# Performance work log

Measured on AMD Instinct MI355X. Metric: run time of the kernel, lower is better.

## Reference

```python
import jax, jax.numpy as jnp
import numpy as np

D_MODEL = 1024
N_HEADS = 16
D_K = D_MODEL // N_HEADS


def _rope_sin_cos(seq_len, d_k, dtype):
    inv_freq = 1.0 / (10000.0 ** (jnp.arange(0, d_k, 2, dtype=jnp.float32) / d_k))
    pos = jnp.arange(seq_len, dtype=jnp.float32)[:, None]          # [S,1]
    ang = pos * inv_freq[None, :]                                   # [S,d_k/2]
    sin = jnp.concatenate([jnp.sin(ang), jnp.sin(ang)], axis=-1)    # [S,d_k]
    cos = jnp.concatenate([jnp.cos(ang), jnp.cos(ang)], axis=-1)
    return sin.astype(dtype), cos.astype(dtype)


def _rotate_half(x):
    x1, x2 = jnp.split(x, 2, axis=-1)
    return jnp.concatenate([-x2, x1], axis=-1)


def _apply_rope(x, sin, cos):
    # x: [B,H,S,d_k]; sin/cos: [S,d_k] broadcast over B,H
    return x * cos[None, None] + _rotate_half(x) * sin[None, None]


def setup_inputs() -> dict:
    key = jax.random.key(0)
    ks = jax.random.split(key, 8)
    B, S = 2, 2048
    s = 1.0 / np.sqrt(D_MODEL)
    return {
        "query": jax.random.normal(ks[0], (B, S, D_MODEL), jnp.float32),
        "key": jax.random.normal(ks[1], (B, S, D_MODEL), jnp.float32),
        "value": jax.random.normal(ks[2], (B, S, D_MODEL), jnp.float32),
        "Wq": jax.random.normal(ks[3], (D_MODEL, D_MODEL), jnp.float32) * s,
        "Wk": jax.random.normal(ks[4], (D_MODEL, D_MODEL), jnp.float32) * s,
        "Wv": jax.random.normal(ks[5], (D_MODEL, D_MODEL), jnp.float32) * s,
        "Wo": jax.random.normal(ks[6], (D_MODEL, D_MODEL), jnp.float32) * s,
        "bo": jnp.zeros((D_MODEL,), jnp.float32),
    }


def reference(query, key, value, Wq, Wk, Wv, Wo, bo):
    B, Sq, _ = query.shape
    Sk = key.shape[1]
    # projections; torch Linear: x @ W.T (here W stored as [out,in])
    Q = (query @ Wq.T).reshape(B, Sq, N_HEADS, D_K).transpose(0, 2, 1, 3)
    K = (key @ Wk.T).reshape(B, Sk, N_HEADS, D_K).transpose(0, 2, 1, 3)
    V = (value @ Wv.T).reshape(B, Sk, N_HEADS, D_K).transpose(0, 2, 1, 3)
    sin_q, cos_q = _rope_sin_cos(Sq, D_K, Q.dtype)
    sin_k, cos_k = _rope_sin_cos(Sk, D_K, K.dtype)
    Q = _apply_rope(Q, sin_q, cos_q)
    K = _apply_rope(K, sin_k, cos_k)
    scores = jnp.einsum("bhqd,bhkd->bhqk", Q, K) / jnp.sqrt(jnp.asarray(D_K, Q.dtype))
    attn = jax.nn.softmax(scores, axis=-1)
    ctx = jnp.einsum("bhqk,bhkd->bhqd", attn, V)
    ctx = ctx.transpose(0, 2, 1, 3).reshape(B, Sq, D_MODEL)
    out = ctx @ Wo.T + bo
    return out, attn
```

## Files before the change

### kernel.cpp

```cpp
#include <hip/hip_runtime.h>
#include <cmath>

#define BB 2
#define SS 2048
#define DMODEL 1024
#define NHEADS 16
#define DK 64
#define BSR (BB*SS)

typedef float f32x4 __attribute__((ext_vector_type(4)));
typedef short s16x8 __attribute__((ext_vector_type(8)));
typedef unsigned short ushort_t;
#define MFMA_BF16 __builtin_amdgcn_mfma_f32_16x16x32_bf16

__device__ __forceinline__ unsigned short f2bf(float x) {
    unsigned int u = __float_as_uint(x);
    unsigned int r = u + 0x7FFFu + ((u >> 16) & 1u);
    return (unsigned short)(r >> 16);
}
__device__ __forceinline__ float bf2f(unsigned short h) {
    return __uint_as_float(((unsigned int)h) << 16);
}
__device__ __forceinline__ unsigned int pk2(float lo, float hi) {
    return (unsigned int)f2bf(lo) | ((unsigned int)f2bf(hi) << 16);
}

__device__ __forceinline__ size_t qk_idx(int bh, int s, int d) {
    return ((((size_t)bh * 128 + (s >> 4)) * 2 + (d >> 5)) * 4 + ((d >> 3) & 3)) * 128
           + (size_t)((s & 15) * 8 + (d & 7));
}
__device__ __forceinline__ size_t v_idx(int bh, int s, int d) {
    return ((((size_t)bh * 64 + (s >> 5)) * 4 + (d >> 4)) * 4 + ((s >> 3) & 3)) * 128
           + (size_t)((d & 15) * 8 + (s & 7));
}

__global__ __launch_bounds__(256)
void split_all(const float* __restrict__ q, const float* __restrict__ k,
               const float* __restrict__ v, const float* __restrict__ wq,
               const float* __restrict__ wk, const float* __restrict__ wv,
               const float* __restrict__ wo,
               ushort_t* qsh, ushort_t* qsl, ushort_t* ksh, ushort_t* ksl,
               ushort_t* vsh, ushort_t* vsl,
               ushort_t* wqh, ushort_t* wql, ushort_t* wkh, ushort_t* wkl,
               ushort_t* wvh, ushort_t* wvl, ushort_t* woh, ushort_t* wol)
{
    int blk = blockIdx.x;
    const float* src; ushort_t* dh; ushort_t* dl;
    if      (blk < 2048) { src = q;  dh = qsh; dl = qsl; }
    else if (blk < 4096) { src = k;  dh = ksh; dl = ksl; blk -= 2048; }
    else if (blk < 6144) { src = v;  dh = vsh; dl = vsl; blk -= 4096; }
    else if (blk < 6656) { src = wq; dh = wqh; dl = wql; blk -= 6144; }
    else if (blk < 7168) { src = wk; dh = wkh; dl = wkl; blk -= 6656; }
    else if (blk < 7680) { src = wv; dh = wvh; dl = wvl; blk -= 7168; }
    else                 { src = wo; dh = woh; dl = wol; blk -= 7680; }
    const size_t off = (size_t)blk * 2048 + threadIdx.x * 8;
    float4 a = *reinterpret_cast<const float4*>(src + off);
    float4 b = *reinterpret_cast<const float4*>(src + off + 4);
    float xs[8] = {a.x, a.y, a.z, a.w, b.x, b.y, b.z, b.w};
    s16x8 hi, lo;
#pragma unroll
    for (int i = 0; i < 8; ++i) {
        unsigned short h = f2bf(xs[i]);
        hi[i] = (short)h;
        lo[i] = (short)f2bf(xs[i] - bf2f(h));
    }
    *reinterpret_cast<s16x8*>(dh + off) = hi;
    *reinterpret_cast<s16x8*>(dl + off) = lo;
}

__global__ __launch_bounds__(256)
void build_tab(float2* __restrict__ tab)
{
    const int t = blockIdx.x * 256 + threadIdx.x;
    const int s = t >> 5, j = t & 31;
    const double l2 = 13.287712379549449 / 32.0;
    const float invf = (float)exp2(-(double)j * l2);
    const float ang = (float)s * invf;
    tab[t] = make_float2(cosf(ang), sinf(ang));
}

template<int MODE>
__global__ __launch_bounds__(256)
void gemm_mfma(const ushort_t* __restrict__ Ah, const ushort_t* __restrict__ Al,
               const ushort_t* __restrict__ Bh, const ushort_t* __restrict__ Bl,
               float* __restrict__ outF, const float* __restrict__ bias,
               ushort_t* __restrict__ O1, ushort_t* __restrict__ O2,
               const float2* __restrict__ tab)
{
    __shared__ __align__(16) ushort_t smAh[128 * 64];
    __shared__ __align__(16) ushort_t smAl[128 * 64];
    __shared__ __align__(16) ushort_t smBh[64 * 64];
    __shared__ __align__(16) ushort_t smBl[64 * 64];

    const int tid = threadIdx.x;
    const int lane = tid & 63;
    const int w = tid >> 6;
    const int lane16 = lane & 15;
    const int grp = (lane >> 4) & 3;
    const int m0 = blockIdx.y * 128;
    const int n0 = blockIdx.x * 64;
    const int K = 1024;

    f32x4 acc[2][4];
#pragma unroll
    for (int a = 0; a < 2; ++a)
#pragma unroll
        for (int e = 0; e < 4; ++e) acc[a][e] = (f32x4){0.f, 0.f, 0.f, 0.f};

    for (int k0 = 0; k0 < K; k0 += 64) {
#pragma unroll
        for (int i = 0; i < 4; ++i) {
            const int c = tid + 256 * i;
            const int row = c >> 3, gs = c & 7;
            const int dst = row * 64 + ((gs ^ (row & 7)) * 8);
            const size_t src = (size_t)(m0 + row) * K + k0 + gs * 8;
            *reinterpret_cast<s16x8*>(&smAh[dst]) = *reinterpret_cast<const s16x8*>(&Ah[src]);
            *reinterpret_cast<s16x8*>(&smAl[dst]) = *reinterpret_cast<const s16x8*>(&Al[src]);
        }
#pragma unroll
        for (int i = 0; i < 2; ++i) {
            const int c = tid + 256 * i;
            const int row = c >> 3, gs = c & 7;
            const int dst = row * 64 + ((gs ^ (row & 7)) * 8);
            const size_t src = (size_t)(n0 + row) * K + k0 + gs * 8;
            *reinterpret_cast<s16x8*>(&smBh[dst]) = *reinterpret_cast<const s16x8*>(&Bh[src]);
            *reinterpret_cast<s16x8*>(&smBl[dst]) = *reinterpret_cast<const s16x8*>(&Bl[src]);
        }
        __syncthreads();
#pragma unroll
        for (int ks = 0; ks < 2; ++ks) {
            const int slotk = ks * 4 + grp;
            s16x8 afh[2], afl[2], bfh[4], bfl[4];
#pragma unroll
            for (int mt = 0; mt < 2; ++mt) {
                const int row = w * 32 + mt * 16 + lane16;
                const int off = row * 64 + ((slotk ^ (row & 7)) * 8);
                afh[mt] = *reinterpret_cast<const s16x8*>(&smAh[off]);
                afl[mt] = *reinterpret_cast<const s16x8*>(&smAl[off]);
            }
#pragma unroll
            for (int nt = 0; nt < 4; ++nt) {
                const int row = nt * 16 + lane16;
                const int off = row * 64 + ((slotk ^ (row & 7)) * 8);
                bfh[nt] = *reinterpret_cast<const s16x8*>(&smBh[off]);
                bfl[nt] = *reinterpret_cast<const s16x8*>(&smBl[off]);
            }
#pragma unroll
            for (int mt = 0; mt < 2; ++mt)
#pragma unroll
                for (int nt = 0; nt < 4; ++nt) {
                    acc[mt][nt] = MFMA_BF16(afh[mt], bfl[nt], acc[mt][nt], 0, 0, 0);
                    acc[mt][nt] = MFMA_BF16(afl[mt], bfh[nt], acc[mt][nt], 0, 0, 0);
                    acc[mt][nt] = MFMA_BF16(afh[mt], bfh[nt], acc[mt][nt], 0, 0, 0);
                }
        }
        __syncthreads();
    }

    if constexpr (MODE == 0) {
#pragma unroll
        for (int mt = 0; mt < 2; ++mt)
#pragma unroll
            for (int r = 0; r < 4; ++r) {
                const int m = m0 + w * 32 + mt * 16 + grp * 4 + r;
#pragma unroll
                for (int nt = 0; nt < 4; ++nt) {
                    const int n = n0 + nt * 16 + lane16;
                    outF[(size_t)m * 1024 + n] = acc[mt][nt][r] + bias[n];
                }
            }
    } else if constexpr (MODE == 1) {
        const int hh = blockIdx.x;
#pragma unroll
        for (int mt = 0; mt < 2; ++mt)
#pragma unroll
            for (int r = 0; r < 4; ++r) {
                const int m = m0 + w * 32 + mt * 16 + grp * 4 + r;
                const int b = m >> 11, s = m & (SS - 1);
                const int bh = b * 16 + hh;
#pragma unroll
                for (int ntp = 0; ntp < 2; ++ntp) {
                    const int j = ntp * 16 + lane16;
                    const float2 cs = tab[s * 32 + j];
                    const float x1 = acc[mt][ntp][r], x2 = acc[mt][ntp + 2][r];
                    const float r1 = x1 * cs.x - x2 * cs.y;
                    const float r2 = x2 * cs.x + x1 * cs.y;
                    const size_t i1 = qk_idx(bh, s, j);
                    const size_t i2 = qk_idx(bh, s, j + 32);
                    const unsigned short h1 = f2bf(r1);
                    O1[i1] = h1;  O2[i1] = f2bf(r1 - bf2f(h1));
                    const unsigned short h2 = f2bf(r2);
                    O1[i2] = h2;  O2[i2] = f2bf(r2 - bf2f(h2));
                }
            }
    } else {
        const int hh = blockIdx.x;
#pragma unroll
        for (int mt = 0; mt < 2; ++mt)
#pragma unroll
            for (int r = 0; r < 4; ++r) {
                const int m = m0 + w * 32 + mt * 16 + grp * 4 + r;
                const int b = m >> 11, s = m & (SS - 1);
                const int bh = b * 16 + hh;
#pragma unroll
                for (int nt = 0; nt < 4; ++nt) {
                    const int d = nt * 16 + lane16;
                    O1[v_idx(bh, s, d)] = f2bf(acc[mt][nt][r]);
                }
            }
    }
}

#define SCALE_L2E 0.180336879f

__global__ __launch_bounds__(1024, 4)
void attn_v6(const ushort_t* __restrict__ Qf_h, const ushort_t* __restrict__ Qf_l,
             const ushort_t* __restrict__ Kf_h, const ushort_t* __restrict__ Kf_l,
             const ushort_t* __restrict__ Vf,
             float* __restrict__ attn, ushort_t* __restrict__ ctxh, ushort_t* __restrict__ ctxl)
{
    __shared__ __align__(16) float slots[8][32][68];
    __shared__ float lsum[16][32];
    __shared__ float rinvS[32];

    const int tid = threadIdx.x;
    const int lane = tid & 63;
    const int w = tid >> 6;
    const int lane16 = lane & 15;
    const int grp = lane >> 4;

    const int bid = blockIdx.x;
    const int idx = bid >> 3;
    const int bh = (bid & 7) * 4 + (idx >> 6);
    const int q0 = (idx & 63) * 32;

    s16x8 qh[2][2], ql[2][2];
#pragma unroll
    for (int qt = 0; qt < 2; ++qt) {
        const size_t qb = ((size_t)(bh * 128 + (q0 >> 4) + qt) * 2) * 512 + lane * 8;
        qh[qt][0] = *reinterpret_cast<const s16x8*>(Qf_h + qb);
        qh[qt][1] = *reinterpret_cast<const s16x8*>(Qf_h + qb + 512);
        ql[qt][0] = *reinterpret_cast<const s16x8*>(Qf_l + qb);
        ql[qt][1] = *reinterpret_cast<const s16x8*>(Qf_l + qb + 512);
    }

    f32x4 p[8][2];
#pragma unroll
    for (int kt = 0; kt < 8; ++kt) {
        const size_t kb = ((size_t)(bh * 128 + w * 8 + kt) * 2) * 512 + lane * 8;
        const s16x8 kh0 = *reinterpret_cast<const s16x8*>(Kf_h + kb);
        const s16x8 kh1 = *reinterpret_cast<const s16x8*>(Kf_h + kb + 512);
        const s16x8 kl0 = *reinterpret_cast<const s16x8*>(Kf_l + kb);
        const s16x8 kl1 = *reinterpret_cast<const s16x8*>(Kf_l + kb + 512);
#pragma unroll
        for (int qt = 0; qt < 2; ++qt) {
            f32x4 t = {0.f, 0.f, 0.f, 0.f};
            t = MFMA_BF16(kh0, ql[qt][0], t, 0, 0, 0);
            t = MFMA_BF16(kh1, ql[qt][1], t, 0, 0, 0);
            t = MFMA_BF16(kl0, qh[qt][0], t, 0, 0, 0);
            t = MFMA_BF16(kl1, qh[qt][1], t, 0, 0, 0);
            t = MFMA_BF16(kh0, qh[qt][0], t, 0, 0, 0);
            t = MFMA_BF16(kh1, qh[qt][1], t, 0, 0, 0);
            p[kt][qt] = t;
        }
    }

    float lq[2] = {0.f, 0.f};
#pragma unroll
    for (int kt = 0; kt < 8; ++kt)
#pragma unroll
        for (int qt = 0; qt < 2; ++qt)
#pragma unroll
            for (int r = 0; r < 4; ++r) {
                const float e = exp2f(p[kt][qt][r] * SCALE_L2E);
                p[kt][qt][r] = e;
                lq[qt] += e;
            }
#pragma unroll
    for (int qt = 0; qt < 2; ++qt) {
        lq[qt] += __shfl_xor(lq[qt], 16, 64);
        lq[qt] += __shfl_xor(lq[qt], 32, 64);
    }
    if (grp == 0) {
        lsum[w][lane16]      = lq[0];
        lsum[w][16 + lane16] = lq[1];
    }
    __syncthreads();
    float tot0 = 0.f, tot1 = 0.f;
#pragma unroll
    for (int w2 = 0; w2 < 16; ++w2) {
        tot0 += lsum[w2][lane16];
        tot1 += lsum[w2][16 + lane16];
    }
    const float rinv[2] = {1.0f / tot0, 1.0f / tot1};
    if (w == 0 && grp == 0) {
        rinvS[lane16]      = rinv[0];
        rinvS[16 + lane16] = rinv[1];
    }

#pragma unroll
    for (int qt = 0; qt < 2; ++qt) {
        const size_t arow = ((size_t)bh * SS + q0 + qt * 16 + lane16) * SS + w * 128 + grp * 4;
#pragma unroll
        for (int kt = 0; kt < 8; ++kt) {
            f32x4 v4;
            v4[0] = p[kt][qt][0] * rinv[qt]; v4[1] = p[kt][qt][1] * rinv[qt];
            v4[2] = p[kt][qt][2] * rinv[qt]; v4[3] = p[kt][qt][3] * rinv[qt];
            *reinterpret_cast<f32x4*>(&attn[arow + kt * 16]) = v4;
        }
    }

    f32x4 acc[4][2];
#pragma unroll
    for (int dt = 0; dt < 4; ++dt) {
        acc[dt][0] = (f32x4){0.f, 0.f, 0.f, 0.f};
        acc[dt][1] = (f32x4){0.f, 0.f, 0.f, 0.f};
    }
    const int src0 = lane16 + ((grp & 1) << 5);
    const int src1 = src0 + 16;
    const bool sel = (grp >> 1) != 0;
#pragma unroll
    for (int kc = 0; kc < 4; ++kc) {
        s16x8 bfr[2];
#pragma unroll
        for (int qt = 0; qt < 2; ++qt) {
            const unsigned int A0 = pk2(p[2*kc][qt][0],   p[2*kc][qt][1]);
            const unsigned int A1 = pk2(p[2*kc][qt][2],   p[2*kc][qt][3]);
            const unsigned int B0 = pk2(p[2*kc+1][qt][0], p[2*kc+1][qt][1]);
            const unsigned int B1 = pk2(p[2*kc+1][qt][2], p[2*kc+1][qt][3]);
            const unsigned int d0a = (unsigned int)__shfl((int)A0, src0, 64);
            const unsigned int d0b = (unsigned int)__shfl((int)B0, src0, 64);
            const unsigned int d1a = (unsigned int)__shfl((int)A1, src0, 64);
            const unsigned int d1b = (unsigned int)__shfl((int)B1, src0, 64);
            const unsigned int d2a = (unsigned int)__shfl((int)A0, src1, 64);
            const unsigned int d2b = (unsigned int)__shfl((int)B0, src1, 64);
            const unsigned int d3a = (unsigned int)__shfl((int)A1, src1, 64);
            const unsigned int d3b = (unsigned int)__shfl((int)B1, src1, 64);
            union { unsigned int u[4]; s16x8 v; } bu;
            bu.u[0] = sel ? d0b : d0a;
            bu.u[1] = sel ? d1b : d1a;
            bu.u[2] = sel ? d2b : d2a;
            bu.u[3] = sel ? d3b : d3a;
            bfr[qt] = bu.v;
        }
#pragma unroll
        for (int dt = 0; dt < 4; ++dt) {
            const s16x8 vf = *reinterpret_cast<const s16x8*>(
                &Vf[((size_t)(bh * 64 + w * 4 + kc) * 4 + dt) * 512 + lane * 8]);
            acc[dt][0] = MFMA_BF16(vf, bfr[0], acc[dt][0], 0, 0, 0);
            acc[dt][1] = MFMA_BF16(vf, bfr[1], acc[dt][1], 0, 0, 0);
        }
    }

    if (w >= 8) {
        float* slot = &slots[w - 8][0][0];
#pragma unroll
        for (int dt = 0; dt < 4; ++dt)
#pragma unroll
            for (int qt = 0; qt < 2; ++qt) {
                f32x4 v4;
                v4[0] = acc[dt][qt][0]; v4[1] = acc[dt][qt][1];
                v4[2] = acc[dt][qt][2]; v4[3] = acc[dt][qt][3];
                *reinterpret_cast<f32x4*>(&slot[(qt * 16 + lane16) * 68 + dt * 16 + grp * 4]) = v4;
            }
    }
    __syncthreads();
    if (w < 8) {
        float* slot = &slots[w][0][0];
#pragma unroll
        for (int dt = 0; dt < 4; ++dt)
#pragma unroll
            for (int qt = 0; qt < 2; ++qt) {
                f32x4* pp = reinterpret_cast<f32x4*>(&slot[(qt * 16 + lane16) * 68 + dt * 16 + grp * 4]);
                f32x4 o = *pp;
                o[0] += acc[dt][qt][0]; o[1] += acc[dt][qt][1];
                o[2] += acc[dt][qt][2]; o[3] += acc[dt][qt][3];
                *pp = o;
            }
    }
    __syncthreads();

    {
        const int b = bh >> 4, h = bh & 15;
        const int q = tid >> 5;
        const int dp = (tid & 31) * 2;
        float s0 = 0.f, s1 = 0.f;
#pragma unroll
        for (int s = 0; s < 8; ++s) {
            const float2 v = *reinterpret_cast<const float2*>(&slots[s][q][dp]);
            s0 += v.x; s1 += v.y;
        }
        const float rv = rinvS[q];
        s0 *= rv; s1 *= rv;
        const size_t co = ((size_t)b * SS + q0 + q) * DMODEL + h * DK + dp;
        const unsigned short h0 = f2bf(s0);
        const unsigned short l0 = f2bf(s0 - bf2f(h0));
        const unsigned short h1 = f2bf(s1);
        const unsigned short l1 = f2bf(s1 - bf2f(h1));
        *reinterpret_cast<unsigned int*>(ctxh + co) = (unsigned int)h0 | ((unsigned int)h1 << 16);
        *reinterpret_cast<unsigned int*>(ctxl + co) = (unsigned int)l0 | ((unsigned int)l1 << 16);
    }
}

extern "C" void kernel_launch(void* const* d_in, const int* in_sizes, int n_in,
                              void* d_out, int out_size, void* d_ws, size_t ws_size,
                              hipStream_t stream)
{
    const float* query = (const float*)d_in[0];
    const float* key   = (const float*)d_in[1];
    const float* value = (const float*)d_in[2];
    const float* Wq    = (const float*)d_in[3];
    const float* Wk    = (const float*)d_in[4];
    const float* Wv    = (const float*)d_in[5];
    const float* Wo    = (const float*)d_in[6];
    const float* bo    = (const float*)d_in[7];

    float* out   = (float*)d_out;
    float* attnO = out + (size_t)BSR * DMODEL;

    const size_t NPROJ = (size_t)BSR * DMODEL;
    const size_t NW    = (size_t)DMODEL * DMODEL;

    char* p = (char*)d_ws;
    float2* tab = (float2*)p;                 p += 1 << 20;
    ushort_t* qsh = (ushort_t*)p;             p += NPROJ * 2;
    ushort_t* qsl = (ushort_t*)p;             p += NPROJ * 2;
    ushort_t* ksh = (ushort_t*)p;             p += NPROJ * 2;
    ushort_t* ksl = (ushort_t*)p;             p += NPROJ * 2;
    ushort_t* vsh = (ushort_t*)p;             p += NPROJ * 2;
    ushort_t* vsl = (ushort_t*)p;             p += NPROJ * 2;
    ushort_t* wqh = (ushort_t*)p;             p += NW * 2;
    ushort_t* wql = (ushort_t*)p;             p += NW * 2;
    ushort_t* wkh = (ushort_t*)p;             p += NW * 2;
    ushort_t* wkl = (ushort_t*)p;             p += NW * 2;
    ushort_t* wvh = (ushort_t*)p;             p += NW * 2;
    ushort_t* wvl = (ushort_t*)p;             p += NW * 2;
    ushort_t* woh = (ushort_t*)p;             p += NW * 2;
    ushort_t* wol = (ushort_t*)p;             p += NW * 2;
    ushort_t* Vt  = (ushort_t*)p;             p += NPROJ * 2;
    ushort_t* Qhi = vsh; ushort_t* Qlo = vsl;
    ushort_t* Khi = qsh; ushort_t* Klo = qsl;
    ushort_t* ctxhC = ksh; ushort_t* ctxlC = ksl;

    split_all<<<8192, 256, 0, stream>>>(query, key, value, Wq, Wk, Wv, Wo,
                                        qsh, qsl, ksh, ksl, vsh, vsl,
                                        wqh, wql, wkh, wkl, wvh, wvl, woh, wol);
    build_tab<<<256, 256, 0, stream>>>(tab);

    const dim3 ggrid(DMODEL / 64, BSR / 128);
    gemm_mfma<2><<<ggrid, 256, 0, stream>>>(vsh, vsl, wvh, wvl, nullptr, nullptr, Vt, nullptr, nullptr);
    gemm_mfma<1><<<ggrid, 256, 0, stream>>>(qsh, qsl, wqh, wql, nullptr, nullptr, Qhi, Qlo, tab);
    gemm_mfma<1><<<ggrid, 256, 0, stream>>>(ksh, ksl, wkh, wkl, nullptr, nullptr, Khi, Klo, tab);

    attn_v6<<<dim3(2048), 1024, 0, stream>>>(Qhi, Qlo, Khi, Klo, Vt, attnO, ctxhC, ctxlC);

    gemm_mfma<0><<<ggrid, 256, 0, stream>>>(ctxhC, ctxlC, woh, wol, out, bo, nullptr, nullptr, nullptr);
}
```

Baseline: 391.6 us.

## Fuse fp32-to-bf16 hi/lo split into GEMM tile loads and enlarge tiles

Removes the separate split kernel that converted the inputs and weights into bf16 hi/lo pairs in global memory. The projection GEMMs now read fp32 activations and weights directly and split them while staging into shared memory, and the output GEMM splits Wo the same way. Tiles grow to 128x128 with 512 threads in a 4x2 wave layout, and the workspace is reorganised with dedicated buffers instead of aliasing. This drops a full write and re-read of the split copies, at the cost of repeating the conversion work on every tile load and using more shared memory per block.

```diff
diff --git a/kernel.cpp b/kernel.cpp
--- a/kernel.cpp
+++ b/kernel.cpp
@@ -10,6 +10,7 @@
 
 typedef float f32x4 __attribute__((ext_vector_type(4)));
 typedef short s16x8 __attribute__((ext_vector_type(8)));
+typedef short s16x4 __attribute__((ext_vector_type(4)));
 typedef unsigned short ushort_t;
 #define MFMA_BF16 __builtin_amdgcn_mfma_f32_16x16x32_bf16
 
@@ -32,40 +33,6 @@
 __device__ __forceinline__ size_t v_idx(int bh, int s, int d) {
     return ((((size_t)bh * 64 + (s >> 5)) * 4 + (d >> 4)) * 4 + ((s >> 3) & 3)) * 128
            + (size_t)((d & 15) * 8 + (s & 7));
-}
-
-__global__ __launch_bounds__(256)
-void split_all(const float* __restrict__ q, const float* __restrict__ k,
-               const float* __restrict__ v, const float* __restrict__ wq,
-               const float* __restrict__ wk, const float* __restrict__ wv,
-               const float* __restrict__ wo,
-               ushort_t* qsh, ushort_t* qsl, ushort_t* ksh, ushort_t* ksl,
-               ushort_t* vsh, ushort_t* vsl,
-               ushort_t* wqh, ushort_t* wql, ushort_t* wkh, ushort_t* wkl,
-               ushort_t* wvh, ushort_t* wvl, ushort_t* woh, ushort_t* wol)
-{
-    int blk = blockIdx.x;
-    const float* src; ushort_t* dh; ushort_t* dl;
-    if      (blk < 2048) { src = q;  dh = qsh; dl = qsl; }
-    else if (blk < 4096) { src = k;  dh = ksh; dl = ksl; blk -= 2048; }
-    else if (blk < 6144) { src = v;  dh = vsh; dl = vsl; blk -= 4096; }
-    else if (blk < 6656) { src = wq; dh = wqh; dl = wql; blk -= 6144; }
-    else if (blk < 7168) { src = wk; dh = wkh; dl = wkl; blk -= 6656; }
-    else if (blk < 7680) { src = wv; dh = wvh; dl = wvl; blk -= 7168; }
-    else                 { src = wo; dh = woh; dl = wol; blk -= 7680; }
-    const size_t off = (size_t)blk * 2048 + threadIdx.x * 8;
-    float4 a = *reinterpret_cast<const float4*>(src + off);
-    float4 b = *reinterpret_cast<const float4*>(src + off + 4);
-    float xs[8] = {a.x, a.y, a.z, a.w, b.x, b.y, b.z, b.w};
-    s16x8 hi, lo;
-#pragma unroll
-    for (int i = 0; i < 8; ++i) {
-        unsigned short h = f2bf(xs[i]);
-        hi[i] = (short)h;
-        lo[i] = (short)f2bf(xs[i] - bf2f(h));
-    }
-    *reinterpret_cast<s16x8*>(dh + off) = hi;
-    *reinterpret_cast<s16x8*>(dl + off) = lo;
 }
 
 __global__ __launch_bounds__(256)
@@ -79,26 +46,28 @@
     tab[t] = make_float2(cosf(ang), sinf(ang));
 }
 
-template<int MODE>
-__global__ __launch_bounds__(256)
-void gemm_mfma(const ushort_t* __restrict__ Ah, const ushort_t* __restrict__ Al,
-               const ushort_t* __restrict__ Bh, const ushort_t* __restrict__ Bl,
+template<int MODE, int AFP32>
+__global__ __launch_bounds__(512, 4)
+void gemm_mfma(const void* __restrict__ Asrc, const void* __restrict__ Alo_,
+               const float* __restrict__ Wsrc,
                float* __restrict__ outF, const float* __restrict__ bias,
                ushort_t* __restrict__ O1, ushort_t* __restrict__ O2,
                const float2* __restrict__ tab)
 {
     __shared__ __align__(16) ushort_t smAh[128 * 64];
     __shared__ __align__(16) ushort_t smAl[128 * 64];
-    __shared__ __align__(16) ushort_t smBh[64 * 64];
-    __shared__ __align__(16) ushort_t smBl[64 * 64];
+    __shared__ __align__(16) ushort_t smBh[128 * 64];
+    __shared__ __align__(16) ushort_t smBl[128 * 64];
 
     const int tid = threadIdx.x;
     const int lane = tid & 63;
     const int w = tid >> 6;
+    const int wm = w >> 1;
+    const int wn = w & 1;
     const int lane16 = lane & 15;
     const int grp = (lane >> 4) & 3;
     const int m0 = blockIdx.y * 128;
-    const int n0 = blockIdx.x * 64;
+    const int n0 = blockIdx.x * 128;
     const int K = 1024;
 
     f32x4 acc[2][4];
@@ -108,23 +77,58 @@
         for (int e = 0; e < 4; ++e) acc[a][e] = (f32x4){0.f, 0.f, 0.f, 0.f};
 
     for (int k0 = 0; k0 < K; k0 += 64) {
+        if constexpr (AFP32) {
+            const float* A = (const float*)Asrc;
+#pragma unroll
+            for (int i = 0; i < 4; ++i) {
+                const int c = i * 512 + tid;
+                const int row = c >> 4;
+                const int kk = (c & 15) * 4;
+                const float4 v = *reinterpret_cast<const float4*>(
+                    &A[(size_t)(m0 + row) * K + k0 + kk]);
+                s16x4 hi, lo;
+                const float xs[4] = {v.x, v.y, v.z, v.w};
+#pragma unroll
+                for (int j = 0; j < 4; ++j) {
+                    const unsigned short h = f2bf(xs[j]);
+                    hi[j] = (short)h;
+                    lo[j] = (short)f2bf(xs[j] - bf2f(h));
+                }
+                const int dst = row * 64 + ((kk >> 3) ^ (row & 7)) * 8 + (kk & 7);
+                *reinterpret_cast<s16x4*>(&smAh[dst]) = hi;
+                *reinterpret_cast<s16x4*>(&smAl[dst]) = lo;
+            }
+        } else {
+            const ushort_t* Ah = (const ushort_t*)Asrc;
+            const ushort_t* Al = (const ushort_t*)Alo_;
+#pragma unroll
+            for (int i = 0; i < 2; ++i) {
+                const int c = i * 512 + tid;
+                const int row = c >> 3, gs = c & 7;
+                const int dst = row * 64 + ((gs ^ (row & 7)) * 8);
+                const size_t src = (size_t)(m0 + row) * K + k0 + gs * 8;
+                *reinterpret_cast<s16x8*>(&smAh[dst]) = *reinterpret_cast<const s16x8*>(&Ah[src]);
+                *reinterpret_cast<s16x8*>(&smAl[dst]) = *reinterpret_cast<const s16x8*>(&Al[src]);
+            }
+        }
 #pragma unroll
         for (int i = 0; i < 4; ++i) {
-            const int c = tid + 256 * i;
-            const int row = c >> 3, gs = c & 7;
-            const int dst = row * 64 + ((gs ^ (row & 7)) * 8);
-            const size_t src = (size_t)(m0 + row) * K + k0 + gs * 8;
-            *reinterpret_cast<s16x8*>(&smAh[dst]) = *reinterpret_cast<const s16x8*>(&Ah[src]);
-            *reinterpret_cast<s16x8*>(&smAl[dst]) = *reinterpret_cast<const s16x8*>(&Al[src]);
-        }
-#pragma unroll
-        for (int i = 0; i < 2; ++i) {
-            const int c = tid + 256 * i;
-            const int row = c >> 3, gs = c & 7;
-            const int dst = row * 64 + ((gs ^ (row & 7)) * 8);
-            const size_t src = (size_t)(n0 + row) * K + k0 + gs * 8;
-            *reinterpret_cast<s16x8*>(&smBh[dst]) = *reinterpret_cast<const s16x8*>(&Bh[src]);
-            *reinterpret_cast<s16x8*>(&smBl[dst]) = *reinterpret_cast<const s16x8*>(&Bl[src]);
+            const int c = i * 512 + tid;
+            const int row = c >> 4;
+            const int kk = (c & 15) * 4;
+            const float4 v = *reinterpret_cast<const float4*>(
+                &Wsrc[(size_t)(n0 + row) * K + k0 + kk]);
+            s16x4 hi, lo;
+            const float xs[4] = {v.x, v.y, v.z, v.w};
+#pragma unroll
+            for (int j = 0; j < 4; ++j) {
+                const unsigned short h = f2bf(xs[j]);
+                hi[j] = (short)h;
+                lo[j] = (short)f2bf(xs[j] - bf2f(h));
+            }
+            const int dst = row * 64 + ((kk >> 3) ^ (row & 7)) * 8 + (kk & 7);
+            *reinterpret_cast<s16x4*>(&smBh[dst]) = hi;
+            *reinterpret_cast<s16x4*>(&smBl[dst]) = lo;
         }
         __syncthreads();
 #pragma unroll
@@ -133,14 +137,14 @@
             s16x8 afh[2], afl[2], bfh[4], bfl[4];
 #pragma unroll
             for (int mt = 0; mt < 2; ++mt) {
-                const int row = w * 32 + mt * 16 + lane16;
+                const int row = wm * 32 + mt * 16 + lane16;
                 const int off = row * 64 + ((slotk ^ (row & 7)) * 8);
                 afh[mt] = *reinterpret_cast<const s16x8*>(&smAh[off]);
                 afl[mt] = *reinterpret_cast<const s16x8*>(&smAl[off]);
             }
 #pragma unroll
             for (int nt = 0; nt < 4; ++nt) {
-                const int row = nt * 16 + lane16;
+                const int row = wn * 64 + nt * 16 + lane16;
                 const int off = row * 64 + ((slotk ^ (row & 7)) * 8);
                 bfh[nt] = *reinterpret_cast<const s16x8*>(&smBh[off]);
                 bfl[nt] = *reinterpret_cast<const s16x8*>(&smBl[off]);
@@ -162,20 +166,20 @@
         for (int mt = 0; mt < 2; ++mt)
 #pragma unroll
             for (int r = 0; r < 4; ++r) {
-                const int m = m0 + w * 32 + mt * 16 + grp * 4 + r;
+                const int m = m0 + wm * 32 + mt * 16 + grp * 4 + r;
 #pragma unroll
                 for (int nt = 0; nt < 4; ++nt) {
-                    const int n = n0 + nt * 16 + lane16;
+                    const int n = n0 + wn * 64 + nt * 16 + lane16;
                     outF[(size_t)m * 1024 + n] = acc[mt][nt][r] + bias[n];
                 }
             }
     } else if constexpr (MODE == 1) {
-        const int hh = blockIdx.x;
+        const int hh = (n0 + wn * 64) >> 6;
 #pragma unroll
         for (int mt = 0; mt < 2; ++mt)
 #pragma unroll
             for (int r = 0; r < 4; ++r) {
-                const int m = m0 + w * 32 + mt * 16 + grp * 4 + r;
+                const int m = m0 + wm * 32 + mt * 16 + grp * 4 + r;
                 const int b = m >> 11, s = m & (SS - 1);
                 const int bh = b * 16 + hh;
 #pragma unroll
@@ -194,12 +198,12 @@
                 }
             }
     } else {
-        const int hh = blockIdx.x;
+        const int hh = (n0 + wn * 64) >> 6;
 #pragma unroll
         for (int mt = 0; mt < 2; ++mt)
 #pragma unroll
             for (int r = 0; r < 4; ++r) {
-                const int m = m0 + w * 32 + mt * 16 + grp * 4 + r;
+                const int m = m0 + wm * 32 + mt * 16 + grp * 4 + r;
                 const int b = m >> 11, s = m & (SS - 1);
                 const int bh = b * 16 + hh;
 #pragma unroll
@@ -419,40 +423,25 @@
     float* attnO = out + (size_t)BSR * DMODEL;
 
     const size_t NPROJ = (size_t)BSR * DMODEL;
-    const size_t NW    = (size_t)DMODEL * DMODEL;
 
     char* p = (char*)d_ws;
     float2* tab = (float2*)p;                 p += 1 << 20;
-    ushort_t* qsh = (ushort_t*)p;             p += NPROJ * 2;
-    ushort_t* qsl = (ushort_t*)p;             p += NPROJ * 2;
-    ushort_t* ksh = (ushort_t*)p;             p += NPROJ * 2;
-    ushort_t* ksl = (ushort_t*)p;             p += NPROJ * 2;
-    ushort_t* vsh = (ushort_t*)p;             p += NPROJ * 2;
-    ushort_t* vsl = (ushort_t*)p;             p += NPROJ * 2;
-    ushort_t* wqh = (ushort_t*)p;             p += NW * 2;
-    ushort_t* wql = (ushort_t*)p;             p += NW * 2;
-    ushort_t* wkh = (ushort_t*)p;             p += NW * 2;
-    ushort_t* wkl = (ushort_t*)p;             p += NW * 2;
-    ushort_t* wvh = (ushort_t*)p;             p += NW * 2;
-    ushort_t* wvl = (ushort_t*)p;             p += NW * 2;
-    ushort_t* woh = (ushort_t*)p;             p += NW * 2;
-    ushort_t* wol = (ushort_t*)p;             p += NW * 2;
+    ushort_t* Qhi = (ushort_t*)p;             p += NPROJ * 2;
+    ushort_t* Qlo = (ushort_t*)p;             p += NPROJ * 2;
+    ushort_t* Khi = (ushort_t*)p;             p += NPROJ * 2;
+    ushort_t* Klo = (ushort_t*)p;             p += NPROJ * 2;
     ushort_t* Vt  = (ushort_t*)p;             p += NPROJ * 2;
-    ushort_t* Qhi = vsh; ushort_t* Qlo = vsl;
-    ushort_t* Khi = qsh; ushort_t* Klo = qsl;
-    ushort_t* ctxhC = ksh; ushort_t* ctxlC = ksl;
-
-    split_all<<<8192, 256, 0, stream>>>(query, key, value, Wq, Wk, Wv, Wo,
-                                        qsh, qsl, ksh, ksl, vsh, vsl,
-                                        wqh, wql, wkh, wkl, wvh, wvl, woh, wol);
+    ushort_t* ctxh = (ushort_t*)p;            p += NPROJ * 2;
+    ushort_t* ctxl = (ushort_t*)p;            p += NPROJ * 2;
+
     build_tab<<<256, 256, 0, stream>>>(tab);
 
-    const dim3 ggrid(DMODEL / 64, BSR / 128);
-    gemm_mfma<2><<<ggrid, 256, 0, stream>>>(vsh, vsl, wvh, wvl, nullptr, nullptr, Vt, nullptr, nullptr);
-    gemm_mfma<1><<<ggrid, 256, 0, stream>>>(qsh, qsl, wqh, wql, nullptr, nullptr, Qhi, Qlo, tab);
-    gemm_mfma<1><<<ggrid, 256, 0, stream>>>(ksh, ksl, wkh, wkl, nullptr, nullptr, Khi, Klo, tab);
-
-    attn_v6<<<dim3(2048), 1024, 0, stream>>>(Qhi, Qlo, Khi, Klo, Vt, attnO, ctxhC, ctxlC);
-
-    gemm_mfma<0><<<ggrid, 256, 0, stream>>>(ctxhC, ctxlC, woh, wol, out, bo, nullptr, nullptr, nullptr);
-}
+    const dim3 ggrid(DMODEL / 128, BSR / 128);
+    gemm_mfma<2, 1><<<ggrid, 512, 0, stream>>>(value, nullptr, Wv, nullptr, nullptr, Vt, nullptr, nullptr);
+    gemm_mfma<1, 1><<<ggrid, 512, 0, stream>>>(query, nullptr, Wq, nullptr, nullptr, Qhi, Qlo, tab);
+    gemm_mfma<1, 1><<<ggrid, 512, 0, stream>>>(key,   nullptr, Wk, nullptr, nullptr, Khi, Klo, tab);
+
+    attn_v6<<<dim3(2048), 1024, 0, stream>>>(Qhi, Qlo, Khi, Klo, Vt, attnO, ctxh, ctxl);
+
+    gemm_mfma<0, 0><<<ggrid, 512, 0, stream>>>(ctxh, ctxl, Wo, out, bo, nullptr, nullptr, nullptr);
+}
```

Result: slower. 551.3 us (+40.8%).

## Widen GEMM tiles to 128x128 and prefetch K while fusing exp and pack in attention

Applied to the files above, without the earlier changes.

The projection and output GEMMs now use 128x128 tiles with 512 threads arranged as a 4x2 wave grid. This halves the block count and doubles the reuse of each loaded A tile. In the attention kernel, K fragments are double-buffered so the next loads are issued ahead of the MFMAs. Exponentials are now computed right after each score tile and packed straight to bf16, which cuts register pressure from the fp32 probability array. The catch is that the stored attention probabilities are now rebuilt from bf16-rounded values, so the attn output loses precision.

```diff
diff --git a/kernel.cpp b/kernel.cpp
--- a/kernel.cpp
+++ b/kernel.cpp
@@ -80,7 +80,7 @@
 }
 
 template<int MODE>
-__global__ __launch_bounds__(256)
+__global__ __launch_bounds__(512, 4)
 void gemm_mfma(const ushort_t* __restrict__ Ah, const ushort_t* __restrict__ Al,
                const ushort_t* __restrict__ Bh, const ushort_t* __restrict__ Bl,
                float* __restrict__ outF, const float* __restrict__ bias,
@@ -89,16 +89,18 @@
 {
     __shared__ __align__(16) ushort_t smAh[128 * 64];
     __shared__ __align__(16) ushort_t smAl[128 * 64];
-    __shared__ __align__(16) ushort_t smBh[64 * 64];
-    __shared__ __align__(16) ushort_t smBl[64 * 64];
+    __shared__ __align__(16) ushort_t smBh[128 * 64];
+    __shared__ __align__(16) ushort_t smBl[128 * 64];
 
     const int tid = threadIdx.x;
     const int lane = tid & 63;
     const int w = tid >> 6;
+    const int wm = w >> 1;
+    const int wn = w & 1;
     const int lane16 = lane & 15;
     const int grp = (lane >> 4) & 3;
     const int m0 = blockIdx.y * 128;
-    const int n0 = blockIdx.x * 64;
+    const int n0 = blockIdx.x * 128;
     const int K = 1024;
 
     f32x4 acc[2][4];
@@ -109,22 +111,16 @@
 
     for (int k0 = 0; k0 < K; k0 += 64) {
 #pragma unroll
-        for (int i = 0; i < 4; ++i) {
-            const int c = tid + 256 * i;
+        for (int i = 0; i < 2; ++i) {
+            const int c = i * 512 + tid;
             const int row = c >> 3, gs = c & 7;
             const int dst = row * 64 + ((gs ^ (row & 7)) * 8);
-            const size_t src = (size_t)(m0 + row) * K + k0 + gs * 8;
-            *reinterpret_cast<s16x8*>(&smAh[dst]) = *reinterpret_cast<const s16x8*>(&Ah[src]);
-            *reinterpret_cast<s16x8*>(&smAl[dst]) = *reinterpret_cast<const s16x8*>(&Al[src]);
-        }
-#pragma unroll
-        for (int i = 0; i < 2; ++i) {
-            const int c = tid + 256 * i;
-            const int row = c >> 3, gs = c & 7;
-            const int dst = row * 64 + ((gs ^ (row & 7)) * 8);
-            const size_t src = (size_t)(n0 + row) * K + k0 + gs * 8;
-            *reinterpret_cast<s16x8*>(&smBh[dst]) = *reinterpret_cast<const s16x8*>(&Bh[src]);
-            *reinterpret_cast<s16x8*>(&smBl[dst]) = *reinterpret_cast<const s16x8*>(&Bl[src]);
+            const size_t srcA = (size_t)(m0 + row) * K + k0 + gs * 8;
+            *reinterpret_cast<s16x8*>(&smAh[dst]) = *reinterpret_cast<const s16x8*>(&Ah[srcA]);
+            *reinterpret_cast<s16x8*>(&smAl[dst]) = *reinterpret_cast<const s16x8*>(&Al[srcA]);
+            const size_t srcB = (size_t)(n0 + row) * K + k0 + gs * 8;
+            *reinterpret_cast<s16x8*>(&smBh[dst]) = *reinterpret_cast<const s16x8*>(&Bh[srcB]);
+            *reinterpret_cast<s16x8*>(&smBl[dst]) = *reinterpret_cast<const s16x8*>(&Bl[srcB]);
         }
         __syncthreads();
 #pragma unroll
@@ -133,14 +129,14 @@
             s16x8 afh[2], afl[2], bfh[4], bfl[4];
 #pragma unroll
             for (int mt = 0; mt < 2; ++mt) {
-                const int row = w * 32 + mt * 16 + lane16;
+                const int row = wm * 32 + mt * 16 + lane16;
                 const int off = row * 64 + ((slotk ^ (row & 7)) * 8);
                 afh[mt] = *reinterpret_cast<const s16x8*>(&smAh[off]);
                 afl[mt] = *reinterpret_cast<const s16x8*>(&smAl[off]);
             }
 #pragma unroll
             for (int nt = 0; nt < 4; ++nt) {
-                const int row = nt * 16 + lane16;
+                const int row = wn * 64 + nt * 16 + lane16;
                 const int off = row * 64 + ((slotk ^ (row & 7)) * 8);
                 bfh[nt] = *reinterpret_cast<const s16x8*>(&smBh[off]);
                 bfl[nt] = *reinterpret_cast<const s16x8*>(&smBl[off]);
@@ -162,20 +158,20 @@
         for (int mt = 0; mt < 2; ++mt)
 #pragma unroll
             for (int r = 0; r < 4; ++r) {
-                const int m = m0 + w * 32 + mt * 16 + grp * 4 + r;
+                const int m = m0 + wm * 32 + mt * 16 + grp * 4 + r;
 #pragma unroll
                 for (int nt = 0; nt < 4; ++nt) {
-                    const int n = n0 + nt * 16 + lane16;
+                    const int n = n0 + wn * 64 + nt * 16 + lane16;
                     outF[(size_t)m * 1024 + n] = acc[mt][nt][r] + bias[n];
                 }
             }
     } else if constexpr (MODE == 1) {
-        const int hh = blockIdx.x;
+        const int hh = (n0 + wn * 64) >> 6;
 #pragma unroll
         for (int mt = 0; mt < 2; ++mt)
 #pragma unroll
             for (int r = 0; r < 4; ++r) {
-                const int m = m0 + w * 32 + mt * 16 + grp * 4 + r;
+                const int m = m0 + wm * 32 + mt * 16 + grp * 4 + r;
                 const int b = m >> 11, s = m & (SS - 1);
                 const int bh = b * 16 + hh;
 #pragma unroll
@@ -194,12 +190,12 @@
                 }
             }
     } else {
-        const int hh = blockIdx.x;
+        const int hh = (n0 + wn * 64) >> 6;
 #pragma unroll
         for (int mt = 0; mt < 2; ++mt)
 #pragma unroll
             for (int r = 0; r < 4; ++r) {
-                const int m = m0 + w * 32 + mt * 16 + grp * 4 + r;
+                const int m = m0 + wm * 32 + mt * 16 + grp * 4 + r;
                 const int b = m >> 11, s = m & (SS - 1);
                 const int bh = b * 16 + hh;
 #pragma unroll
@@ -214,7 +210,7 @@
 #define SCALE_L2E 0.180336879f
 
 __global__ __launch_bounds__(1024, 4)
-void attn_v6(const ushort_t* __restrict__ Qf_h, const ushort_t* __restrict__ Qf_l,
+void attn_v7(const ushort_t* __restrict__ Qf_h, const ushort_t* __restrict__ Qf_l,
              const ushort_t* __restrict__ Kf_h, const ushort_t* __restrict__ Kf_l,
              const ushort_t* __restrict__ Vf,
              float* __restrict__ attn, ushort_t* __restrict__ ctxh, ushort_t* __restrict__ ctxl)
@@ -244,14 +240,31 @@
         ql[qt][1] = *reinterpret_cast<const s16x8*>(Qf_l + qb + 512);
     }
 
-    f32x4 p[8][2];
+    unsigned int pp[8][2][2];
+    float lq[2] = {0.f, 0.f};
+    s16x8 kbuf[2][4];
+#pragma unroll
+    for (int s = 0; s < 2; ++s) {
+        const size_t kb = ((size_t)(bh * 128 + w * 8 + s) * 2) * 512 + lane * 8;
+        kbuf[s][0] = *reinterpret_cast<const s16x8*>(Kf_h + kb);
+        kbuf[s][1] = *reinterpret_cast<const s16x8*>(Kf_h + kb + 512);
+        kbuf[s][2] = *reinterpret_cast<const s16x8*>(Kf_l + kb);
+        kbuf[s][3] = *reinterpret_cast<const s16x8*>(Kf_l + kb + 512);
+    }
 #pragma unroll
     for (int kt = 0; kt < 8; ++kt) {
-        const size_t kb = ((size_t)(bh * 128 + w * 8 + kt) * 2) * 512 + lane * 8;
-        const s16x8 kh0 = *reinterpret_cast<const s16x8*>(Kf_h + kb);
-        const s16x8 kh1 = *reinterpret_cast<const s16x8*>(Kf_h + kb + 512);
-        const s16x8 kl0 = *reinterpret_cast<const s16x8*>(Kf_l + kb);
-        const s16x8 kl1 = *reinterpret_cast<const s16x8*>(Kf_l + kb + 512);
+        s16x8 nh0, nh1, nl0, nl1;
+        if (kt < 6) {
+            const size_t kn = ((size_t)(bh * 128 + w * 8 + kt + 2) * 2) * 512 + lane * 8;
+            nh0 = *reinterpret_cast<const s16x8*>(Kf_h + kn);
+            nh1 = *reinterpret_cast<const s16x8*>(Kf_h + kn + 512);
+            nl0 = *reinterpret_cast<const s16x8*>(Kf_l + kn);
+            nl1 = *reinterpret_cast<const s16x8*>(Kf_l + kn + 512);
+        }
+        const s16x8 kh0 = kbuf[kt & 1][0];
+        const s16x8 kh1 = kbuf[kt & 1][1];
+        const s16x8 kl0 = kbuf[kt & 1][2];
+        const s16x8 kl1 = kbuf[kt & 1][3];
 #pragma unroll
         for (int qt = 0; qt < 2; ++qt) {
             f32x4 t = {0.f, 0.f, 0.f, 0.f};
@@ -261,21 +274,20 @@
             t = MFMA_BF16(kl1, qh[qt][1], t, 0, 0, 0);
             t = MFMA_BF16(kh0, qh[qt][0], t, 0, 0, 0);
             t = MFMA_BF16(kh1, qh[qt][1], t, 0, 0, 0);
-            p[kt][qt] = t;
-        }
-    }
-
-    float lq[2] = {0.f, 0.f};
-#pragma unroll
-    for (int kt = 0; kt < 8; ++kt)
-#pragma unroll
-        for (int qt = 0; qt < 2; ++qt)
-#pragma unroll
-            for (int r = 0; r < 4; ++r) {
-                const float e = exp2f(p[kt][qt][r] * SCALE_L2E);
-                p[kt][qt][r] = e;
-                lq[qt] += e;
-            }
+            const float e0 = exp2f(t[0] * SCALE_L2E);
+            const float e1 = exp2f(t[1] * SCALE_L2E);
+            const float e2 = exp2f(t[2] * SCALE_L2E);
+            const float e3 = exp2f(t[3] * SCALE_L2E);
+            lq[qt] += e0; lq[qt] += e1; lq[qt] += e2; lq[qt] += e3;
+            pp[kt][qt][0] = pk2(e0, e1);
+            pp[kt][qt][1] = pk2(e2, e3);
+        }
+        if (kt < 6) {
+            kbuf[kt & 1][0] = nh0; kbuf[kt & 1][1] = nh1;
+            kbuf[kt & 1][2] = nl0; kbuf[kt & 1][3] = nl1;
+        }
+    }
+
 #pragma unroll
     for (int qt = 0; qt < 2; ++qt) {
         lq[qt] += __shfl_xor(lq[qt], 16, 64);
@@ -303,9 +315,13 @@
         const size_t arow = ((size_t)bh * SS + q0 + qt * 16 + lane16) * SS + w * 128 + grp * 4;
 #pragma unroll
         for (int kt = 0; kt < 8; ++kt) {
+            const unsigned int u0 = pp[kt][qt][0];
+            const unsigned int u1 = pp[kt][qt][1];
             f32x4 v4;
-            v4[0] = p[kt][qt][0] * rinv[qt]; v4[1] = p[kt][qt][1] * rinv[qt];
-            v4[2] = p[kt][qt][2] * rinv[qt]; v4[3] = p[kt][qt][3] * rinv[qt];
+            v4[0] = __uint_as_float(u0 << 16) * rinv[qt];
+            v4[1] = __uint_as_float(u0 & 0xffff0000u) * rinv[qt];
+            v4[2] = __uint_as_float(u1 << 16) * rinv[qt];
+            v4[3] = __uint_as_float(u1 & 0xffff0000u) * rinv[qt];
             *reinterpret_cast<f32x4*>(&attn[arow + kt * 16]) = v4;
         }
     }
@@ -324,10 +340,10 @@
         s16x8 bfr[2];
 #pragma unroll
         for (int qt = 0; qt < 2; ++qt) {
-            const unsigned int A0 = pk2(p[2*kc][qt][0],   p[2*kc][qt][1]);
-            const unsigned int A1 = pk2(p[2*kc][qt][2],   p[2*kc][qt][3]);
-            const unsigned int B0 = pk2(p[2*kc+1][qt][0], p[2*kc+1][qt][1]);
-            const unsigned int B1 = pk2(p[2*kc+1][qt][2], p[2*kc+1][qt][3]);
+            const unsigned int A0 = pp[2 * kc][qt][0];
+            const unsigned int A1 = pp[2 * kc][qt][1];
+            const unsigned int B0 = pp[2 * kc + 1][qt][0];
+            const unsigned int B1 = pp[2 * kc + 1][qt][1];
             const unsigned int d0a = (unsigned int)__shfl((int)A0, src0, 64);
             const unsigned int d0b = (unsigned int)__shfl((int)B0, src0, 64);
             const unsigned int d1a = (unsigned int)__shfl((int)A1, src0, 64);
@@ -371,11 +387,11 @@
         for (int dt = 0; dt < 4; ++dt)
 #pragma unroll
             for (int qt = 0; qt < 2; ++qt) {
-                f32x4* pp = reinterpret_cast<f32x4*>(&slot[(qt * 16 + lane16) * 68 + dt * 16 + grp * 4]);
-                f32x4 o = *pp;
+                f32x4* pq = reinterpret_cast<f32x4*>(&slot[(qt * 16 + lane16) * 68 + dt * 16 + grp * 4]);
+                f32x4 o = *pq;
                 o[0] += acc[dt][qt][0]; o[1] += acc[dt][qt][1];
                 o[2] += acc[dt][qt][2]; o[3] += acc[dt][qt][3];
-                *pp = o;
+                *pq = o;
             }
     }
     __syncthreads();
@@ -447,12 +463,12 @@
                                         wqh, wql, wkh, wkl, wvh, wvl, woh, wol);
     build_tab<<<256, 256, 0, stream>>>(tab);
 
-    const dim3 ggrid(DMODEL / 64, BSR / 128);
-    gemm_mfma<2><<<ggrid, 256, 0, stream>>>(vsh, vsl, wvh, wvl, nullptr, nullptr, Vt, nullptr, nullptr);
-    gemm_mfma<1><<<ggrid, 256, 0, stream>>>(qsh, qsl, wqh, wql, nullptr, nullptr, Qhi, Qlo, tab);
-    gemm_mfma<1><<<ggrid, 256, 0, stream>>>(ksh, ksl, wkh, wkl, nullptr, nullptr, Khi, Klo, tab);
-
-    attn_v6<<<dim3(2048), 1024, 0, stream>>>(Qhi, Qlo, Khi, Klo, Vt, attnO, ctxhC, ctxlC);
-
-    gemm_mfma<0><<<ggrid, 256, 0, stream>>>(ctxhC, ctxlC, woh, wol, out, bo, nullptr, nullptr, nullptr);
-}
+    const dim3 ggrid(DMODEL / 128, BSR / 128);
+    gemm_mfma<2><<<ggrid, 512, 0, stream>>>(vsh, vsl, wvh, wvl, nullptr, nullptr, Vt, nullptr, nullptr);
+    gemm_mfma<1><<<ggrid, 512, 0, stream>>>(qsh, qsl, wqh, wql, nullptr, nullptr, Qhi, Qlo, tab);
+    gemm_mfma<1><<<ggrid, 512, 0, stream>>>(ksh, ksl, wkh, wkl, nullptr, nullptr, Khi, Klo, tab);
+
+    attn_v7<<<dim3(2048), 1024, 0, stream>>>(Qhi, Qlo, Khi, Klo, Vt, attnO, ctxhC, ctxlC);
+
+    gemm_mfma<0><<<ggrid, 512, 0, stream>>>(ctxhC, ctxlC, woh, wol, out, bo, nullptr, nullptr, nullptr);
+}
```

Result: slower. 432.0 us (+10.3%).
